# Optimization experiments

Measured on AMD Instinct MI355X. Metric: run time of the kernel, lower is better.

The kernel has to match this reference:

```python
import jax, jax.numpy as jnp
import numpy as np

INPUT_DIM, HIDDEN, NUM_CLASSES = 16, 128, 24
B, T = 4096, 1024  # raw I/Q frame (B, 2, T); seq_len = 2*T/INPUT_DIM = 128


def setup_inputs() -> dict:
    key = jax.random.key(0)
    ks = jax.random.split(key, 12)
    s = 1.0 / np.sqrt(HIDDEN)  # torch default uniform bound ~ use scaled normal
    def w(k, shape, scale):
        return jax.random.normal(k, shape, jnp.float32) * scale
    return {
        "x": jax.random.normal(ks[0], (B, 2, T), jnp.float32),
        "w_ih1": w(ks[1], (3 * HIDDEN, INPUT_DIM), s),
        "w_hh1": w(ks[2], (3 * HIDDEN, HIDDEN), s),
        "b_ih1": w(ks[3], (3 * HIDDEN,), s),
        "b_hh1": w(ks[4], (3 * HIDDEN,), s),
        "w_ih2": w(ks[5], (3 * HIDDEN, HIDDEN), s),
        "w_hh2": w(ks[6], (3 * HIDDEN, HIDDEN), s),
        "b_ih2": w(ks[7], (3 * HIDDEN,), s),
        "b_hh2": w(ks[8], (3 * HIDDEN,), s),
        "fc_w": w(ks[9], (NUM_CLASSES, HIDDEN), s),
        "fc_b": w(ks[10], (NUM_CLASSES,), s),
    }


def _gru_layer(x, w_ih, w_hh, b_ih, b_hh, return_seq=True):
    # x: (B, L, D). PyTorch GRU gate order: r, z, n.
    Bb = x.shape[0]
    H = w_hh.shape[1]
    xp = jnp.einsum('bld,gd->blg', x, w_ih) + b_ih  # (B, L, 3H) precomputed input proj

    def step(h, xt):
        gh = h @ w_hh.T + b_hh  # (B, 3H)
        ir, iz, inn = jnp.split(xt, 3, axis=-1)
        hr, hz, hn = jnp.split(gh, 3, axis=-1)
        r = jax.nn.sigmoid(ir + hr)
        z = jax.nn.sigmoid(iz + hz)
        n = jnp.tanh(inn + r * hn)
        h_new = (1.0 - z) * n + z * h
        return h_new, (h_new if return_seq else 0.0)

    h0 = jnp.zeros((Bb, H), x.dtype)
    h_last, ys = jax.lax.scan(step, h0, jnp.swapaxes(xp, 0, 1))
    if return_seq:
        return jnp.swapaxes(ys, 0, 1)
    return h_last


def reference(x, w_ih1, w_hh1, b_ih1, b_hh1, w_ih2, w_hh2, b_ih2, b_hh2, fc_w, fc_b):
    Bb = x.shape[0]
    # (B,2,T) -> (B,2,L,8) -> (B,L,2,8) -> (B,L,16)
    h = x.reshape(Bb, 2, -1, INPUT_DIM // 2)
    h = jnp.swapaxes(h, 1, 2).reshape(Bb, -1, INPUT_DIM)
    seq1 = _gru_layer(h, w_ih1, w_hh1, b_ih1, b_hh1, return_seq=True)
    last = _gru_layer(seq1, w_ih2, w_hh2, b_ih2, b_hh2, return_seq=False)
    return last @ fc_w.T + fc_b
```

## Files before the change

kernel.cpp:

```cpp
#include <hip/hip_runtime.h>


typedef _Float16 half_t;
typedef _Float16 half8 __attribute__((ext_vector_type(8)));
typedef _Float16 half4v __attribute__((ext_vector_type(4)));
typedef float f32x4 __attribute__((ext_vector_type(4)));

#define BB 16
#define HS 136
#define XS 520

static __device__ __forceinline__ f32x4 mfma16(half8 a, half8 b, f32x4 c) {
  return __builtin_amdgcn_mfma_f32_16x16x32_f16(a, b, c, 0, 0, 0);
}

static __device__ __forceinline__ void pin(half8& v) {
  f32x4 t = __builtin_bit_cast(f32x4, v);
  asm volatile("" : "+v"(t));
  v = __builtin_bit_cast(half8, t);
}

static __device__ __forceinline__ half8 zero8() {
  half8 v;
#pragma unroll
  for (int i = 0; i < 8; ++i) v[i] = (half_t)0.f;
  return v;
}

static __device__ __forceinline__ half8 ldw8(const float* __restrict__ p) {
  float4 a = *(const float4*)p;
  float4 b = *(const float4*)(p + 4);
  half8 r;
  r[0] = (half_t)a.x; r[1] = (half_t)a.y; r[2] = (half_t)a.z; r[3] = (half_t)a.w;
  r[4] = (half_t)b.x; r[5] = (half_t)b.y; r[6] = (half_t)b.z; r[7] = (half_t)b.w;
  return r;
}

static __device__ __forceinline__ float sigm(float v) {
  return __builtin_amdgcn_rcpf(1.f + __expf(-v));
}
static __device__ __forceinline__ float tanh_fast(float v) {
  float e = __expf(2.f * v);
  return 1.f - 2.f * __builtin_amdgcn_rcpf(1.f + e);
}

__global__ __launch_bounds__(512, 2) void gru_fused(
    const float* __restrict__ x,
    const float* __restrict__ wih1, const float* __restrict__ whh1,
    const float* __restrict__ bih1, const float* __restrict__ bhh1,
    const float* __restrict__ wih2, const float* __restrict__ whh2,
    const float* __restrict__ bih2, const float* __restrict__ bhh2,
    const float* __restrict__ fcw, const float* __restrict__ fcb,
    float* __restrict__ out)
{
  __shared__ __align__(16) half_t xl[BB][XS];
  __shared__ __align__(16) half_t h1b[2][BB][HS];
  __shared__ __align__(16) half_t h2b[2][BB][HS];
  __shared__ float h2f[BB][129];

  const int tid = threadIdx.x;
  const int lane = tid & 63;
  const int wv = tid >> 6;
  const int q = lane >> 4;
  const int c = lane & 15;
  const int jc = wv * 16 + c;
  const int s0 = blockIdx.x * BB;

  for (int i = tid; i < 2 * BB * HS; i += 512) {
    ((half_t*)h1b)[i] = (half_t)0.f;
    ((half_t*)h2b)[i] = (half_t)0.f;
  }

  const float b1r  = bih1[jc]       + bhh1[jc];
  const float b1z  = bih1[128 + jc] + bhh1[128 + jc];
  const float b1in = bih1[256 + jc];
  const float b1hn = bhh1[256 + jc];
  const float b2r  = bih2[jc]       + bhh2[jc];
  const float b2z  = bih2[128 + jc] + bhh2[128 + jc];
  const float b2in = bih2[256 + jc];
  const float b2hn = bhh2[256 + jc];

  half8 wi1r, wi1z, wi1n;
  if (q < 2) {
    wi1r = ldw8(wih1 + (0 * 128 + jc) * 16 + q * 8);
    wi1z = ldw8(wih1 + (1 * 128 + jc) * 16 + q * 8);
    wi1n = ldw8(wih1 + (2 * 128 + jc) * 16 + q * 8);
  } else {
    wi1r = zero8(); wi1z = zero8(); wi1n = zero8();
  }
  pin(wi1r); pin(wi1z); pin(wi1n);

  half8 wh1r[4], wh1z[4], wh1n[4], wi2r[4], wi2z[4], wi2n[4], wh2r[4], wh2z[4], wh2n[4];
#pragma unroll
  for (int kk = 0; kk < 4; ++kk) {
    const int ko = kk * 32 + q * 8;
    wh1r[kk] = ldw8(whh1 + (0 * 128 + jc) * 128 + ko);
    wh1z[kk] = ldw8(whh1 + (1 * 128 + jc) * 128 + ko);
    wh1n[kk] = ldw8(whh1 + (2 * 128 + jc) * 128 + ko);
    wi2r[kk] = ldw8(wih2 + (0 * 128 + jc) * 128 + ko);
    wi2z[kk] = ldw8(wih2 + (1 * 128 + jc) * 128 + ko);
    wi2n[kk] = ldw8(wih2 + (2 * 128 + jc) * 128 + ko);
    wh2r[kk] = ldw8(whh2 + (0 * 128 + jc) * 128 + ko);
    wh2z[kk] = ldw8(whh2 + (1 * 128 + jc) * 128 + ko);
    wh2n[kk] = ldw8(whh2 + (2 * 128 + jc) * 128 + ko);
    pin(wh1r[kk]); pin(wh1z[kk]); pin(wh1n[kk]);
    pin(wi2r[kk]); pin(wi2z[kk]); pin(wi2n[kk]);
    pin(wh2r[kk]); pin(wh2z[kk]); pin(wh2n[kk]);
  }

  float h1p[4] = {0.f, 0.f, 0.f, 0.f};
  float h2p[4] = {0.f, 0.f, 0.f, 0.f};

  for (int tc = 0; tc < 4; ++tc) {
#pragma unroll
    for (int it = 0; it < 4; ++it) {
      int idx = tid + it * 512;
      int s = idx >> 7;
      int rem = idx & 127;
      int ch = rem >> 6;
      int i4 = rem & 63;
      const float4 v = *(const float4*)(x + (size_t)(s0 + s) * 2048 + ch * 1024 + tc * 256 + i4 * 4);
      half4v hv;
      hv[0] = (half_t)v.x; hv[1] = (half_t)v.y; hv[2] = (half_t)v.z; hv[3] = (half_t)v.w;
      *(half4v*)&xl[s][(i4 >> 1) * 16 + ch * 8 + (i4 & 1) * 4] = hv;
    }
    __syncthreads();

    for (int tt = 0; tt < 32; ++tt) {
      const int i = tc * 32 + tt;
      const int rb = i & 1;
      const int wb = rb ^ 1;

      f32x4 ar  = {b1r, b1r, b1r, b1r};
      f32x4 az  = {b1z, b1z, b1z, b1z};
      f32x4 ain = {b1in, b1in, b1in, b1in};
      f32x4 ahn = {b1hn, b1hn, b1hn, b1hn};
      f32x4 cr  = {b2r, b2r, b2r, b2r};
      f32x4 cz  = {b2z, b2z, b2z, b2z};
      f32x4 cin = {b2in, b2in, b2in, b2in};
      f32x4 chn = {b2hn, b2hn, b2hn, b2hn};

      {
        half8 ax = zero8();
        if (q < 2) ax = *(const half8*)&xl[c][tt * 16 + q * 8];
        ar  = mfma16(ax, wi1r, ar);
        az  = mfma16(ax, wi1z, az);
        ain = mfma16(ax, wi1n, ain);
      }
#pragma unroll
      for (int kk = 0; kk < 4; ++kk) {
        half8 ah = *(const half8*)&h1b[rb][c][kk * 32 + q * 8];
        half8 a2 = *(const half8*)&h2b[rb][c][kk * 32 + q * 8];
        ar  = mfma16(ah, wh1r[kk], ar);
        az  = mfma16(ah, wh1z[kk], az);
        ahn = mfma16(ah, wh1n[kk], ahn);
        cr  = mfma16(ah, wi2r[kk], cr);
        cz  = mfma16(ah, wi2z[kk], cz);
        cin = mfma16(ah, wi2n[kk], cin);
        cr  = mfma16(a2, wh2r[kk], cr);
        cz  = mfma16(a2, wh2z[kk], cz);
        chn = mfma16(a2, wh2n[kk], chn);
      }

#pragma unroll
      for (int r = 0; r < 4; ++r) {
        float rg = sigm(ar[r]);
        float zg = sigm(az[r]);
        float ng = tanh_fast(fmaf(rg, ahn[r], ain[r]));
        float hn = fmaf(zg, h1p[r] - ng, ng);
        h1p[r] = hn;
        h1b[wb][q * 4 + r][jc] = (half_t)hn;
      }
      if (i > 0) {
#pragma unroll
        for (int r = 0; r < 4; ++r) {
          float rg = sigm(cr[r]);
          float zg = sigm(cz[r]);
          float ng = tanh_fast(fmaf(rg, chn[r], cin[r]));
          float hn = fmaf(zg, h2p[r] - ng, ng);
          h2p[r] = hn;
          h2b[wb][q * 4 + r][jc] = (half_t)hn;
        }
      }
      __syncthreads();
    }
  }

  {
    f32x4 cr  = {b2r, b2r, b2r, b2r};
    f32x4 cz  = {b2z, b2z, b2z, b2z};
    f32x4 cin = {b2in, b2in, b2in, b2in};
    f32x4 chn = {b2hn, b2hn, b2hn, b2hn};
#pragma unroll
    for (int kk = 0; kk < 4; ++kk) {
      half8 a1 = *(const half8*)&h1b[0][c][kk * 32 + q * 8];
      half8 a2 = *(const half8*)&h2b[0][c][kk * 32 + q * 8];
      cr  = mfma16(a1, wi2r[kk], cr);
      cz  = mfma16(a1, wi2z[kk], cz);
      cin = mfma16(a1, wi2n[kk], cin);
      cr  = mfma16(a2, wh2r[kk], cr);
      cz  = mfma16(a2, wh2z[kk], cz);
      chn = mfma16(a2, wh2n[kk], chn);
    }
#pragma unroll
    for (int r = 0; r < 4; ++r) {
      float rg = sigm(cr[r]);
      float zg = sigm(cz[r]);
      float ng = tanh_fast(fmaf(rg, chn[r], cin[r]));
      h2p[r] = fmaf(zg, h2p[r] - ng, ng);
    }
  }

#pragma unroll
  for (int r = 0; r < 4; ++r) h2f[q * 4 + r][jc] = h2p[r];
  __syncthreads();
  if (tid < 384) {
    const int m = tid & 15;
    const int cls = tid >> 4;
    const float* w = fcw + cls * 128;
    float acc = fcb[cls];
#pragma unroll 8
    for (int j = 0; j < 128; ++j) acc = fmaf(h2f[m][j], w[j], acc);
    out[(size_t)(s0 + m) * 24 + cls] = acc;
  }
}

extern "C" void kernel_launch(void* const* d_in, const int* in_sizes, int n_in,
                              void* d_out, int out_size, void* d_ws, size_t ws_size,
                              hipStream_t stream) {
  (void)in_sizes; (void)n_in; (void)d_ws; (void)ws_size; (void)out_size;
  const float* x    = (const float*)d_in[0];
  const float* wih1 = (const float*)d_in[1];
  const float* whh1 = (const float*)d_in[2];
  const float* bih1 = (const float*)d_in[3];
  const float* bhh1 = (const float*)d_in[4];
  const float* wih2 = (const float*)d_in[5];
  const float* whh2 = (const float*)d_in[6];
  const float* bih2 = (const float*)d_in[7];
  const float* bhh2 = (const float*)d_in[8];
  const float* fcw  = (const float*)d_in[9];
  const float* fcb  = (const float*)d_in[10];
  float* outp = (float*)d_out;
  gru_fused<<<dim3(256), dim3(512), 0, stream>>>(
      x, wih1, whh1, bih1, bhh1, wih2, whh2, bih2, bhh2, fcw, fcb, outp);
}
```

Measured before the change: 282.0 us.

## Fold log2e into weights and share reciprocals across gate activations

Pre-scales the fp16 weight registers by -log2(e) or 2*log2(e) so the gates can use raw exp2, and turns the r/z biases into multiplicative factors applied after the exponential. One reciprocal now serves both the r and z sigmoids, and one serves a pair of tanh evaluations. MFMA accumulators start from zero instead of bias vectors, the layer-2 branch is replaced by a multiplicative mask, and the time loop is unrolled by two. The goal is fewer transcendental and reciprocal instructions on the serial recurrence. In exchange, products of two denominators can overflow and the scaled fp16 weights lose a little precision.

```diff
diff --git a/kernel.cpp b/kernel.cpp
--- a/kernel.cpp
+++ b/kernel.cpp
@@ -10,6 +10,9 @@
 #define HS 136
 #define XS 520
 
+#define NL2E (-1.442695041f)
+#define L2E2 (2.885390082f)
+
 static __device__ __forceinline__ f32x4 mfma16(half8 a, half8 b, f32x4 c) {
   return __builtin_amdgcn_mfma_f32_16x16x32_f16(a, b, c, 0, 0, 0);
 }
@@ -27,22 +30,19 @@
   return v;
 }
 
-static __device__ __forceinline__ half8 ldw8(const float* __restrict__ p) {
+static __device__ __forceinline__ half8 ldw8s(const float* __restrict__ p, float s) {
   float4 a = *(const float4*)p;
   float4 b = *(const float4*)(p + 4);
   half8 r;
-  r[0] = (half_t)a.x; r[1] = (half_t)a.y; r[2] = (half_t)a.z; r[3] = (half_t)a.w;
-  r[4] = (half_t)b.x; r[5] = (half_t)b.y; r[6] = (half_t)b.z; r[7] = (half_t)b.w;
+  r[0] = (half_t)(a.x * s); r[1] = (half_t)(a.y * s);
+  r[2] = (half_t)(a.z * s); r[3] = (half_t)(a.w * s);
+  r[4] = (half_t)(b.x * s); r[5] = (half_t)(b.y * s);
+  r[6] = (half_t)(b.z * s); r[7] = (half_t)(b.w * s);
   return r;
 }
 
-static __device__ __forceinline__ float sigm(float v) {
-  return __builtin_amdgcn_rcpf(1.f + __expf(-v));
-}
-static __device__ __forceinline__ float tanh_fast(float v) {
-  float e = __expf(2.f * v);
-  return 1.f - 2.f * __builtin_amdgcn_rcpf(1.f + e);
-}
+static __device__ __forceinline__ float ex2(float x) { return __builtin_amdgcn_exp2f(x); }
+static __device__ __forceinline__ float rcpa(float x) { return __builtin_amdgcn_rcpf(x); }
 
 __global__ __launch_bounds__(512, 2) void gru_fused(
     const float* __restrict__ x,
@@ -71,20 +71,20 @@
     ((half_t*)h2b)[i] = (half_t)0.f;
   }
 
-  const float b1r  = bih1[jc]       + bhh1[jc];
-  const float b1z  = bih1[128 + jc] + bhh1[128 + jc];
-  const float b1in = bih1[256 + jc];
-  const float b1hn = bhh1[256 + jc];
-  const float b2r  = bih2[jc]       + bhh2[jc];
-  const float b2z  = bih2[128 + jc] + bhh2[128 + jc];
-  const float b2in = bih2[256 + jc];
-  const float b2hn = bhh2[256 + jc];
+  const float eb1r = ex2(NL2E * (bih1[jc] + bhh1[jc]));
+  const float eb1z = ex2(NL2E * (bih1[128 + jc] + bhh1[128 + jc]));
+  const float b1in = L2E2 * bih1[256 + jc];
+  const float b1hn = L2E2 * bhh1[256 + jc];
+  const float eb2r = ex2(NL2E * (bih2[jc] + bhh2[jc]));
+  const float eb2z = ex2(NL2E * (bih2[128 + jc] + bhh2[128 + jc]));
+  const float b2in = L2E2 * bih2[256 + jc];
+  const float b2hn = L2E2 * bhh2[256 + jc];
 
   half8 wi1r, wi1z, wi1n;
   if (q < 2) {
-    wi1r = ldw8(wih1 + (0 * 128 + jc) * 16 + q * 8);
-    wi1z = ldw8(wih1 + (1 * 128 + jc) * 16 + q * 8);
-    wi1n = ldw8(wih1 + (2 * 128 + jc) * 16 + q * 8);
+    wi1r = ldw8s(wih1 + (0 * 128 + jc) * 16 + q * 8, NL2E);
+    wi1z = ldw8s(wih1 + (1 * 128 + jc) * 16 + q * 8, NL2E);
+    wi1n = ldw8s(wih1 + (2 * 128 + jc) * 16 + q * 8, L2E2);
   } else {
     wi1r = zero8(); wi1z = zero8(); wi1n = zero8();
   }
@@ -94,15 +94,15 @@
 #pragma unroll
   for (int kk = 0; kk < 4; ++kk) {
     const int ko = kk * 32 + q * 8;
-    wh1r[kk] = ldw8(whh1 + (0 * 128 + jc) * 128 + ko);
-    wh1z[kk] = ldw8(whh1 + (1 * 128 + jc) * 128 + ko);
-    wh1n[kk] = ldw8(whh1 + (2 * 128 + jc) * 128 + ko);
-    wi2r[kk] = ldw8(wih2 + (0 * 128 + jc) * 128 + ko);
-    wi2z[kk] = ldw8(wih2 + (1 * 128 + jc) * 128 + ko);
-    wi2n[kk] = ldw8(wih2 + (2 * 128 + jc) * 128 + ko);
-    wh2r[kk] = ldw8(whh2 + (0 * 128 + jc) * 128 + ko);
-    wh2z[kk] = ldw8(whh2 + (1 * 128 + jc) * 128 + ko);
-    wh2n[kk] = ldw8(whh2 + (2 * 128 + jc) * 128 + ko);
+    wh1r[kk] = ldw8s(whh1 + (0 * 128 + jc) * 128 + ko, NL2E);
+    wh1z[kk] = ldw8s(whh1 + (1 * 128 + jc) * 128 + ko, NL2E);
+    wh1n[kk] = ldw8s(whh1 + (2 * 128 + jc) * 128 + ko, L2E2);
+    wi2r[kk] = ldw8s(wih2 + (0 * 128 + jc) * 128 + ko, NL2E);
+    wi2z[kk] = ldw8s(wih2 + (1 * 128 + jc) * 128 + ko, NL2E);
+    wi2n[kk] = ldw8s(wih2 + (2 * 128 + jc) * 128 + ko, L2E2);
+    wh2r[kk] = ldw8s(whh2 + (0 * 128 + jc) * 128 + ko, NL2E);
+    wh2z[kk] = ldw8s(whh2 + (1 * 128 + jc) * 128 + ko, NL2E);
+    wh2n[kk] = ldw8s(whh2 + (2 * 128 + jc) * 128 + ko, L2E2);
     pin(wh1r[kk]); pin(wh1z[kk]); pin(wh1n[kk]);
     pin(wi2r[kk]); pin(wi2z[kk]); pin(wi2n[kk]);
     pin(wh2r[kk]); pin(wh2z[kk]); pin(wh2n[kk]);
@@ -111,6 +111,7 @@
   float h1p[4] = {0.f, 0.f, 0.f, 0.f};
   float h2p[4] = {0.f, 0.f, 0.f, 0.f};
 
+#pragma unroll 1
   for (int tc = 0; tc < 4; ++tc) {
 #pragma unroll
     for (int it = 0; it < 4; ++it) {
@@ -126,29 +127,33 @@
     }
     __syncthreads();
 
+#pragma unroll 2
     for (int tt = 0; tt < 32; ++tt) {
       const int i = tc * 32 + tt;
       const int rb = i & 1;
       const int wb = rb ^ 1;
-
-      f32x4 ar  = {b1r, b1r, b1r, b1r};
-      f32x4 az  = {b1z, b1z, b1z, b1z};
-      f32x4 ain = {b1in, b1in, b1in, b1in};
-      f32x4 ahn = {b1hn, b1hn, b1hn, b1hn};
-      f32x4 cr  = {b2r, b2r, b2r, b2r};
-      f32x4 cz  = {b2z, b2z, b2z, b2z};
-      f32x4 cin = {b2in, b2in, b2in, b2in};
-      f32x4 chn = {b2hn, b2hn, b2hn, b2hn};
-
-      {
-        half8 ax = zero8();
-        if (q < 2) ax = *(const half8*)&xl[c][tt * 16 + q * 8];
-        ar  = mfma16(ax, wi1r, ar);
-        az  = mfma16(ax, wi1z, az);
-        ain = mfma16(ax, wi1n, ain);
-      }
-#pragma unroll
-      for (int kk = 0; kk < 4; ++kk) {
+      const float l2m = (i > 0) ? 1.f : 0.f;
+      const f32x4 kZ = {0.f, 0.f, 0.f, 0.f};
+
+      half8 ax = zero8();
+      if (q < 2) ax = *(const half8*)&xl[c][tt * 16 + q * 8];
+      half8 ah0 = *(const half8*)&h1b[rb][c][q * 8];
+      half8 a20 = *(const half8*)&h2b[rb][c][q * 8];
+
+      f32x4 ar  = mfma16(ax, wi1r, kZ);
+      f32x4 az  = mfma16(ax, wi1z, kZ);
+      f32x4 ain = mfma16(ax, wi1n, kZ);
+      f32x4 ahn = mfma16(ah0, wh1n[0], kZ);
+      ar = mfma16(ah0, wh1r[0], ar);
+      az = mfma16(ah0, wh1z[0], az);
+      f32x4 cr  = mfma16(ah0, wi2r[0], kZ);
+      f32x4 cz  = mfma16(ah0, wi2z[0], kZ);
+      f32x4 cin = mfma16(ah0, wi2n[0], kZ);
+      f32x4 chn = mfma16(a20, wh2n[0], kZ);
+      cr = mfma16(a20, wh2r[0], cr);
+      cz = mfma16(a20, wh2z[0], cz);
+#pragma unroll
+      for (int kk = 1; kk < 4; ++kk) {
         half8 ah = *(const half8*)&h1b[rb][c][kk * 32 + q * 8];
         half8 a2 = *(const half8*)&h2b[rb][c][kk * 32 + q * 8];
         ar  = mfma16(ah, wh1r[kk], ar);
@@ -162,37 +167,64 @@
         chn = mfma16(a2, wh2n[kk], chn);
       }
 
+      float C1[4], rg1[4], zg1[4], C2[4], rg2[4], zg2[4];
 #pragma unroll
       for (int r = 0; r < 4; ++r) {
-        float rg = sigm(ar[r]);
-        float zg = sigm(az[r]);
-        float ng = tanh_fast(fmaf(rg, ahn[r], ain[r]));
-        float hn = fmaf(zg, h1p[r] - ng, ng);
-        h1p[r] = hn;
-        h1b[wb][q * 4 + r][jc] = (half_t)hn;
-      }
-      if (i > 0) {
-#pragma unroll
-        for (int r = 0; r < 4; ++r) {
-          float rg = sigm(cr[r]);
-          float zg = sigm(cz[r]);
-          float ng = tanh_fast(fmaf(rg, chn[r], cin[r]));
-          float hn = fmaf(zg, h2p[r] - ng, ng);
-          h2p[r] = hn;
-          h2b[wb][q * 4 + r][jc] = (half_t)hn;
-        }
+        float er = ex2(ar[r]);
+        float ez = ex2(az[r]);
+        float A  = fmaf(er, eb1r, 1.f);
+        float Bv = fmaf(ez, eb1z, 1.f);
+        float R  = rcpa(A * Bv);
+        rg1[r] = R * Bv; zg1[r] = R * A;
+        float av = fmaf(rg1[r], ahn[r] + b1hn, ain[r] + b1in);
+        C1[r] = 1.f + ex2(av);
+      }
+#pragma unroll
+      for (int r = 0; r < 4; ++r) {
+        float er = ex2(cr[r]);
+        float ez = ex2(cz[r]);
+        float A  = fmaf(er, eb2r, 1.f);
+        float Bv = fmaf(ez, eb2z, 1.f);
+        float R  = rcpa(A * Bv);
+        rg2[r] = R * Bv; zg2[r] = R * A;
+        float av = fmaf(rg2[r], chn[r] + b2hn, cin[r] + b2in);
+        C2[r] = 1.f + ex2(av);
+      }
+#pragma unroll
+      for (int p = 0; p < 4; p += 2) {
+        float R1 = rcpa(C1[p] * C1[p + 1]);
+        float n0 = fmaf(R1 * C1[p + 1], -2.f, 1.f);
+        float n1 = fmaf(R1 * C1[p],     -2.f, 1.f);
+        float e0 = fmaf(zg1[p],     h1p[p]     - n0, n0);
+        float e1 = fmaf(zg1[p + 1], h1p[p + 1] - n1, n1);
+        h1p[p] = e0; h1p[p + 1] = e1;
+        h1b[wb][q * 4 + p][jc]     = (half_t)e0;
+        h1b[wb][q * 4 + p + 1][jc] = (half_t)e1;
+        float R2 = rcpa(C2[p] * C2[p + 1]);
+        float m0 = fmaf(R2 * C2[p + 1], -2.f, 1.f);
+        float m1 = fmaf(R2 * C2[p],     -2.f, 1.f);
+        float g0 = fmaf(zg2[p],     h2p[p]     - m0, m0) * l2m;
+        float g1 = fmaf(zg2[p + 1], h2p[p + 1] - m1, m1) * l2m;
+        h2p[p] = g0; h2p[p + 1] = g1;
+        h2b[wb][q * 4 + p][jc]     = (half_t)g0;
+        h2b[wb][q * 4 + p + 1][jc] = (half_t)g1;
       }
       __syncthreads();
     }
   }
 
   {
-    f32x4 cr  = {b2r, b2r, b2r, b2r};
-    f32x4 cz  = {b2z, b2z, b2z, b2z};
-    f32x4 cin = {b2in, b2in, b2in, b2in};
-    f32x4 chn = {b2hn, b2hn, b2hn, b2hn};
-#pragma unroll
-    for (int kk = 0; kk < 4; ++kk) {
+    const f32x4 kZ = {0.f, 0.f, 0.f, 0.f};
+    half8 a10 = *(const half8*)&h1b[0][c][q * 8];
+    half8 a20 = *(const half8*)&h2b[0][c][q * 8];
+    f32x4 cr  = mfma16(a10, wi2r[0], kZ);
+    f32x4 cz  = mfma16(a10, wi2z[0], kZ);
+    f32x4 cin = mfma16(a10, wi2n[0], kZ);
+    f32x4 chn = mfma16(a20, wh2n[0], kZ);
+    cr = mfma16(a20, wh2r[0], cr);
+    cz = mfma16(a20, wh2z[0], cz);
+#pragma unroll
+    for (int kk = 1; kk < 4; ++kk) {
       half8 a1 = *(const half8*)&h1b[0][c][kk * 32 + q * 8];
       half8 a2 = *(const half8*)&h2b[0][c][kk * 32 + q * 8];
       cr  = mfma16(a1, wi2r[kk], cr);
@@ -202,12 +234,25 @@
       cz  = mfma16(a2, wh2z[kk], cz);
       chn = mfma16(a2, wh2n[kk], chn);
     }
+    float C2[4], rg2[4], zg2[4];
 #pragma unroll
     for (int r = 0; r < 4; ++r) {
-      float rg = sigm(cr[r]);
-      float zg = sigm(cz[r]);
-      float ng = tanh_fast(fmaf(rg, chn[r], cin[r]));
-      h2p[r] = fmaf(zg, h2p[r] - ng, ng);
+      float er = ex2(cr[r]);
+      float ez = ex2(cz[r]);
+      float A  = fmaf(er, eb2r, 1.f);
+      float Bv = fmaf(ez, eb2z, 1.f);
+      float R  = rcpa(A * Bv);
+      rg2[r] = R * Bv; zg2[r] = R * A;
+      float av = fmaf(rg2[r], chn[r] + b2hn, cin[r] + b2in);
+      C2[r] = 1.f + ex2(av);
+    }
+#pragma unroll
+    for (int p = 0; p < 4; p += 2) {
+      float R2 = rcpa(C2[p] * C2[p + 1]);
+      float m0 = fmaf(R2 * C2[p + 1], -2.f, 1.f);
+      float m1 = fmaf(R2 * C2[p],     -2.f, 1.f);
+      h2p[p]     = fmaf(zg2[p],     h2p[p]     - m0, m0);
+      h2p[p + 1] = fmaf(zg2[p + 1], h2p[p + 1] - m1, m1);
     }
   }
 
```

After: 261.7 us. 1.08x faster.
